# Performance work log

Measured on AMD Instinct MI355X. Metric: run time of the kernel, lower is better.

Reference implementation:

```python
import jax, jax.numpy as jnp
import numpy as np
import math

D_MODEL = 2048
N_HEADS = 16
HEAD_DIM = D_MODEL // N_HEADS
ROPE_THETA = 10000.0
EPS = 1e-5


def _rope_cos_sin(seq_len, dim, theta):
    inv_freq = 1.0 / theta ** (jnp.arange(0, dim, 2, dtype=jnp.float32) / dim)  # [dim/2]
    t = jnp.arange(seq_len, dtype=jnp.float32)
    freqs = jnp.outer(t, inv_freq)  # [S, dim/2]
    return jnp.cos(freqs), jnp.sin(freqs)


def _apply_rope(x, cos, sin):
    # x: [B, S, H, D]; pairs (even, odd) rotated by angle freqs[s, d/2]
    xs = x.reshape(x.shape[:-1] + (x.shape[-1] // 2, 2))
    x0, x1 = xs[..., 0], xs[..., 1]
    c = cos[None, :, None, :]
    s = sin[None, :, None, :]
    out = jnp.stack([x0 * c - x1 * s, x0 * s + x1 * c], axis=-1)
    return out.reshape(x.shape)


def _layernorm(x, w, eps):
    # LayerNorm over last dim, no bias
    mu = jnp.mean(x, axis=-1, keepdims=True)
    var = jnp.mean(jnp.square(x - mu), axis=-1, keepdims=True)
    return (x - mu) * jax.lax.rsqrt(var + eps) * w


def setup_inputs() -> dict:
    key = jax.random.key(0)
    ks = jax.random.split(key, 5)
    B, S = 2, 2048
    w_std = math.sqrt(1.0 / D_MODEL)  # ~xavier for square matrices
    return {
        "x": jax.random.normal(ks[0], (B, S, D_MODEL), dtype=jnp.float32),
        "wq": jax.random.normal(ks[1], (D_MODEL, D_MODEL), dtype=jnp.float32) * w_std,
        "wk": jax.random.normal(ks[2], (D_MODEL, D_MODEL), dtype=jnp.float32) * w_std,
        "wv": jax.random.normal(ks[3], (D_MODEL, D_MODEL), dtype=jnp.float32) * w_std,
        "wo": jax.random.normal(ks[4], (D_MODEL, D_MODEL), dtype=jnp.float32) * w_std,
        "q_norm_w": jnp.ones((HEAD_DIM,), dtype=jnp.float32),
        "k_norm_w": jnp.ones((HEAD_DIM,), dtype=jnp.float32),
        "window_size": 1024,
    }


def reference(x, wq, wk, wv, wo, q_norm_w, k_norm_w, window_size):
    B, S, _ = x.shape
    # bias-free projections (torch Linear: x @ W.T)
    q = (x @ wq.T).reshape(B, S, N_HEADS, HEAD_DIM)
    k = (x @ wk.T).reshape(B, S, N_HEADS, HEAD_DIM)
    v = (x @ wv.T).reshape(B, S, N_HEADS, HEAD_DIM)

    cos, sin = _rope_cos_sin(S, HEAD_DIM, ROPE_THETA)
    q = _apply_rope(q, cos, sin)
    k = _apply_rope(k, cos, sin)

    # per-head QK LayerNorm (no bias)
    q = _layernorm(q, q_norm_w, EPS)
    k = _layernorm(k, k_norm_w, EPS)

    scale = 1.0 / math.sqrt(HEAD_DIM)
    scores = jnp.einsum("bqhd,bkhd->bhqk", q, k) * scale  # [B,H,S,S]

    # sliding-window causal mask: attend to j in [i - window, i]
    i = jnp.arange(S)[:, None]
    j = jnp.arange(S)[None, :]
    allowed = (j <= i) & (j >= i - window_size)
    scores = jnp.where(allowed, scores, -jnp.inf)

    attn = jax.nn.softmax(scores, axis=-1)
    out = jnp.einsum("bhqk,bkhd->bqhd", attn, v).reshape(B, S, D_MODEL)
    return out @ wo.T
```

## Files before the change

### kernel.cpp

```cpp
#include <hip/hip_runtime.h>

typedef __bf16 bfv8 __attribute__((ext_vector_type(8)));
typedef float f32x4 __attribute__((ext_vector_type(4)));

#define DMODEL 2048
#define NHEADS 16
#define HEADD 128
#define SEQ 2048
#define BATCH 2
#define MROWS (BATCH * SEQ)

__device__ __forceinline__ unsigned short f2bf(float f) {
    unsigned int x = __float_as_uint(f);
    x += 0x7fffu + ((x >> 16) & 1u);
    return (unsigned short)(x >> 16);
}
__device__ __forceinline__ unsigned int pk2(float a, float b) {
    return (unsigned int)f2bf(a) | ((unsigned int)f2bf(b) << 16);
}

__global__ __launch_bounds__(256) void cvt_all(const float* __restrict__ x,
                                               const float* __restrict__ wq,
                                               const float* __restrict__ wk,
                                               const float* __restrict__ wv,
                                               const float* __restrict__ wo,
                                               unsigned short* __restrict__ dst) {
    int bid = blockIdx.x;
    const float* s;
    int off;
    if (bid < 8192)       { s = x;  off = bid; }
    else if (bid < 12288) { s = wq; off = bid - 8192; }
    else if (bid < 16384) { s = wk; off = bid - 12288; }
    else if (bid < 20480) { s = wv; off = bid - 16384; }
    else                  { s = wo; off = bid - 20480; }
    int i = off * 1024 + threadIdx.x * 4;
    float4 v = *(const float4*)(s + i);
    ushort4 o;
    o.x = f2bf(v.x); o.y = f2bf(v.y); o.z = f2bf(v.z); o.w = f2bf(v.w);
    *(ushort4*)(dst + (size_t)bid * 1024 + threadIdx.x * 4) = o;
}

template <int CPRL, int ITERS>
__device__ __forceinline__ void stage_n(const unsigned short* __restrict__ gbase,
                                        unsigned short* lds, size_t strideShorts,
                                        int wave, int lane) {
#pragma unroll
    for (int i = 0; i < ITERS; ++i) {
        int L = wave * (64 * ITERS) + i * 64 + lane;
        int m = L >> CPRL, c = L & ((1 << CPRL) - 1);
        int g = c ^ (m & 7);
        const unsigned short* gp = gbase + (size_t)m * strideShorts + g * 8;
        __builtin_amdgcn_global_load_lds(
            (const __attribute__((address_space(1))) unsigned int*)gp,
            (__attribute__((address_space(3))) unsigned int*)(lds + (size_t)(wave * (64 * ITERS) + i * 64) * 8),
            16, 0, 0);
    }
}

#define GBK 64

__global__ __launch_bounds__(256, 4) void gemm_qkv(const unsigned short* __restrict__ A,
                                                   const unsigned short* __restrict__ Bw,
                                                   unsigned short* __restrict__ Qb,
                                                   unsigned short* __restrict__ Kb,
                                                   unsigned short* __restrict__ VT,
                                                   const float* __restrict__ qnw,
                                                   const float* __restrict__ knw) {
    __shared__ __align__(16) unsigned short As[128 * 64];
    __shared__ __align__(16) unsigned short Bs[128 * 64];
    const int K = DMODEL;
    int tid  = threadIdx.x;
    int bm   = blockIdx.y * 128, bn = blockIdx.x * 128;
    int wave = tid >> 6, lane = tid & 63;
    int wm   = (wave >> 1) * 64, wn = (wave & 1) * 64;
    int lr   = lane & 15, lg = lane >> 4;

    f32x4 acc[4][4];
    f32x4 z = {0.f, 0.f, 0.f, 0.f};
#pragma unroll
    for (int i = 0; i < 4; ++i)
#pragma unroll
        for (int j = 0; j < 4; ++j) acc[i][j] = z;

    const unsigned short* Ab = A  + (size_t)bm * K;
    const unsigned short* Bb = Bw + (size_t)bn * K;

    for (int k0 = 0; k0 < K; k0 += GBK) {
        __syncthreads();
        stage_n<3, 4>(Ab + k0, As, K, wave, lane);
        stage_n<3, 4>(Bb + k0, Bs, K, wave, lane);
        __syncthreads();
#pragma unroll
        for (int kk = 0; kk < GBK; kk += 32) {
            int ck = (kk >> 3) + lg;
            bfv8 af[4], bf[4];
#pragma unroll
            for (int i = 0; i < 4; ++i)
                af[i] = *(const bfv8*)&As[(wm + i * 16 + lr) * 64 + (ck ^ (lr & 7)) * 8];
#pragma unroll
            for (int j = 0; j < 4; ++j)
                bf[j] = *(const bfv8*)&Bs[(wn + j * 16 + lr) * 64 + (ck ^ (lr & 7)) * 8];
#pragma unroll
            for (int i = 0; i < 4; ++i)
#pragma unroll
                for (int j = 0; j < 4; ++j)
                    acc[i][j] = __builtin_amdgcn_mfma_f32_16x16x32_bf16(af[i], bf[j], acc[i][j], 0, 0, 0);
        }
    }
    int lm = lr;
    int region = bn >> 11;
    int nloc   = bn & 2047;
    if (region < 2) {
        unsigned short* C = region ? Kb : Qb;
        const float* nw = region ? knw : qnw;
        float scale = region ? 1.0f : 0.08838834764831845f;
        float invf[4], wnw[4];
#pragma unroll
        for (int j = 0; j < 4; ++j) {
            int dd = wn + j * 16 + lm;
            invf[j] = exp2f(-(float)(dd >> 1) * 0.20762050593046f);
            wnw[j] = nw[dd];
        }
        int sbase = (bm & (SEQ - 1)) + wm + lg * 4;
#pragma unroll
        for (int i = 0; i < 4; ++i)
#pragma unroll
            for (int r = 0; r < 4; ++r) {
                float sv = (float)(sbase + i * 16 + r);
#pragma unroll
                for (int j = 0; j < 4; ++j) {
                    float sn, cs;
                    __sincosf(sv * invf[j], &sn, &cs);
                    float x0 = acc[i][j][r];
                    float x1 = __shfl_xor(x0, 1);
                    acc[i][j][r] = (lm & 1) ? fmaf(x1, sn, x0 * cs)
                                            : fmaf(x0, cs, -(x1 * sn));
                }
            }
        float* red = (float*)As;
        int half = wn >> 6;
        __syncthreads();
#pragma unroll
        for (int i = 0; i < 4; ++i)
#pragma unroll
            for (int r = 0; r < 4; ++r) {
                float a0 = acc[i][0][r], a1 = acc[i][1][r], a2 = acc[i][2][r], a3 = acc[i][3][r];
                float s1 = (a0 + a1) + (a2 + a3);
                float s2 = fmaf(a0, a0, fmaf(a1, a1, fmaf(a2, a2, a3 * a3)));
#pragma unroll
                for (int msk = 1; msk <= 8; msk <<= 1) {
                    s1 += __shfl_xor(s1, msk);
                    s2 += __shfl_xor(s2, msk);
                }
                if (lm == 0) {
                    int rloc = wm + lg * 4 + i * 16 + r;
                    red[(rloc * 2 + half) * 2 + 0] = s1;
                    red[(rloc * 2 + half) * 2 + 1] = s2;
                }
            }
        __syncthreads();
#pragma unroll
        for (int i = 0; i < 4; ++i)
#pragma unroll
            for (int r = 0; r < 4; ++r) {
                int rloc = wm + lg * 4 + i * 16 + r;
                float t1 = red[(rloc * 2 + 0) * 2 + 0] + red[(rloc * 2 + 1) * 2 + 0];
                float t2 = red[(rloc * 2 + 0) * 2 + 1] + red[(rloc * 2 + 1) * 2 + 1];
                float mu  = t1 * (1.0f / 128.0f);
                float var = t2 * (1.0f / 128.0f) - mu * mu;
                float rs  = rsqrtf(var + 1e-5f) * scale;
                size_t rowoff = (size_t)(bm + rloc) * DMODEL + nloc;
#pragma unroll
                for (int j = 0; j < 4; ++j)
                    C[rowoff + wn + j * 16 + lm] = f2bf((acc[i][j][r] - mu) * rs * wnw[j]);
            }
    } else {
        int orow0 = bm + wm + lg * 4;
#pragma unroll
        for (int i = 0; i < 4; ++i) {
            int row = orow0 + i * 16;
            int bb = row >> 11, ss = row & (SEQ - 1);
#pragma unroll
            for (int j = 0; j < 4; ++j) {
                int col = nloc + wn + j * 16 + lm;
                int hh = col >> 7, dd = col & (HEADD - 1);
                ushort4 o4;
                o4.x = f2bf(acc[i][j][0]);
                o4.y = f2bf(acc[i][j][1]);
                o4.z = f2bf(acc[i][j][2]);
                o4.w = f2bf(acc[i][j][3]);
                *(ushort4*)(VT + ((size_t)((bb * NHEADS + hh) * HEADD + dd)) * SEQ + ss) = o4;
            }
        }
    }
}

__global__ __launch_bounds__(256) void gemm_bt(const unsigned short* __restrict__ A,
                                               const unsigned short* __restrict__ Bw,
                                               float* __restrict__ C,
                                               int M, int N, int K) {
    __shared__ __align__(16) unsigned short As[128 * 64];
    __shared__ __align__(16) unsigned short Bs[128 * 64];
    int tid  = threadIdx.x;
    int bm   = blockIdx.y * 128, bn = blockIdx.x * 128;
    int wave = tid >> 6, lane = tid & 63;
    int wm   = (wave >> 1) * 64, wn = (wave & 1) * 64;
    int lr   = lane & 15, lg = lane >> 4;

    f32x4 acc[4][4];
    f32x4 z = {0.f, 0.f, 0.f, 0.f};
#pragma unroll
    for (int i = 0; i < 4; ++i)
#pragma unroll
        for (int j = 0; j < 4; ++j) acc[i][j] = z;

    const unsigned short* Ab = A  + (size_t)bm * K;
    const unsigned short* Bb = Bw + (size_t)bn * K;

    for (int k0 = 0; k0 < K; k0 += GBK) {
        __syncthreads();
        stage_n<3, 4>(Ab + k0, As, K, wave, lane);
        stage_n<3, 4>(Bb + k0, Bs, K, wave, lane);
        __syncthreads();
#pragma unroll
        for (int kk = 0; kk < GBK; kk += 32) {
            int ck = (kk >> 3) + lg;
            bfv8 af[4], bf[4];
#pragma unroll
            for (int i = 0; i < 4; ++i)
                af[i] = *(const bfv8*)&As[(wm + i * 16 + lr) * 64 + (ck ^ (lr & 7)) * 8];
#pragma unroll
            for (int j = 0; j < 4; ++j)
                bf[j] = *(const bfv8*)&Bs[(wn + j * 16 + lr) * 64 + (ck ^ (lr & 7)) * 8];
#pragma unroll
            for (int i = 0; i < 4; ++i)
#pragma unroll
                for (int j = 0; j < 4; ++j)
                    acc[i][j] = __builtin_amdgcn_mfma_f32_16x16x32_bf16(af[i], bf[j], acc[i][j], 0, 0, 0);
        }
    }
    int orow0 = bm + wm + lg * 4;
    int ocol0 = bn + wn + lr;
#pragma unroll
    for (int i = 0; i < 4; ++i)
#pragma unroll
        for (int j = 0; j < 4; ++j)
#pragma unroll
            for (int r = 0; r < 4; ++r)
                C[(size_t)(orow0 + i * 16 + r) * N + ocol0 + j * 16] = acc[i][j][r];
}

#define AQT 128
#define AKT 128

__global__ __launch_bounds__(256, 2) void attn_mfma(const unsigned short* __restrict__ qb,
                                                    const unsigned short* __restrict__ kb,
                                                    const unsigned short* __restrict__ vt,
                                                    unsigned short* __restrict__ ob,
                                                    const int* __restrict__ wptr) {
    __shared__ __align__(16) unsigned short Ks[128 * 128];
    __shared__ __align__(16) unsigned short Ps[4 * 32 * 128];
    int tid  = threadIdx.x;
    int wq   = tid >> 6, lane = tid & 63;
    int lm   = lane & 15, lg = lane >> 4;
    int lm7  = lm & 7;
    int gid  = blockIdx.x;
    int xcd  = gid & 7, slot = gid >> 3;
    int bh   = xcd * 4 + (slot >> 4);
    int b    = bh >> 4, h = bh & 15;
    int q0   = (15 - (slot & 15)) * AQT;
    int W    = *wptr;
    unsigned short* PsW = &Ps[wq * 32 * 128];

    bfv8 qa[2][4];
#pragma unroll
    for (int nq = 0; nq < 2; ++nq) {
        const unsigned short* qp = qb + (size_t)(b * SEQ + q0 + wq * 32 + nq * 16 + lm) * DMODEL + h * HEADD + lg * 8;
#pragma unroll
        for (int kk = 0; kk < 4; ++kk) qa[nq][kk] = *(const bfv8*)(qp + kk * 32);
    }

    f32x4 o[2][8];
    f32x4 z = {0.f, 0.f, 0.f, 0.f};
#pragma unroll
    for (int mq = 0; mq < 2; ++mq)
#pragma unroll
        for (int n = 0; n < 8; ++n) o[mq][n] = z;
    float mrow[2] = {-1e30f, -1e30f}, lrow[2] = {0.f, 0.f};

    const unsigned short* kbase = kb + (size_t)(b * SEQ) * DMODEL + h * HEADD;
    const unsigned short* vbase = vt + (size_t)((b * NHEADS + h) * HEADD) * SEQ;

    int kt_lo = max(0, q0 - W) & ~(AKT - 1);
    int qi0 = q0 + wq * 32 + lm;

    for (int kt = kt_lo; kt < q0 + AQT; kt += AKT) {
        __syncthreads();
        stage_n<4, 8>(kbase + (size_t)kt * DMODEL, Ks, DMODEL, wq, lane);
        __syncthreads();

        f32x4 s[8][2];
#pragma unroll
        for (int j = 0; j < 8; ++j) { s[j][0] = z; s[j][1] = z; }
#pragma unroll
        for (int kk = 0; kk < 4; ++kk)
#pragma unroll
            for (int j = 0; j < 8; ++j) {
                bfv8 af = *(const bfv8*)&Ks[(j * 16 + lm) * 128 + (((kk * 4 + lg)) ^ lm7) * 8];
                s[j][0] = __builtin_amdgcn_mfma_f32_16x16x32_bf16(af, qa[0][kk], s[j][0], 0, 0, 0);
                s[j][1] = __builtin_amdgcn_mfma_f32_16x16x32_bf16(af, qa[1][kk], s[j][1], 0, 0, 0);
            }
        if ((kt + AKT - 1 > q0) || (kt < q0 + AQT - 1 - W)) {
#pragma unroll
            for (int j = 0; j < 8; ++j) {
                int kj0 = kt + j * 16 + lg * 4;
#pragma unroll
                for (int nq = 0; nq < 2; ++nq) {
                    int qi = qi0 + nq * 16;
#pragma unroll
                    for (int r = 0; r < 4; ++r) {
                        bool ok = (kj0 + r <= qi) && (kj0 + r >= qi - W);
                        s[j][nq][r] = ok ? s[j][nq][r] : -1e30f;
                    }
                }
            }
        }
        float alpha[2];
#pragma unroll
        for (int nq = 0; nq < 2; ++nq) {
            float mx = -1e30f;
#pragma unroll
            for (int j = 0; j < 8; ++j)
#pragma unroll
                for (int r = 0; r < 4; ++r) mx = fmaxf(mx, s[j][nq][r]);
            mx = fmaxf(mx, __shfl_xor(mx, 16));
            mx = fmaxf(mx, __shfl_xor(mx, 32));
            float mnew = fmaxf(mrow[nq], mx);
            alpha[nq] = __expf(mrow[nq] - mnew);
            mrow[nq] = mnew;
            float ls = 0.f;
#pragma unroll
            for (int j = 0; j < 8; ++j) {
                float p0 = __expf(s[j][nq][0] - mnew);
                float p1 = __expf(s[j][nq][1] - mnew);
                float p2 = __expf(s[j][nq][2] - mnew);
                float p3 = __expf(s[j][nq][3] - mnew);
                ls += (p0 + p1) + (p2 + p3);
                int c0 = (j * 2 + (lg >> 1)) ^ lm7;
                uint2 wv;
                wv.x = pk2(p0, p1);
                wv.y = pk2(p2, p3);
                *(uint2*)&PsW[(nq * 16 + lm) * 128 + c0 * 8 + (lg & 1) * 4] = wv;
            }
            ls += __shfl_xor(ls, 16);
            ls += __shfl_xor(ls, 32);
            lrow[nq] = lrow[nq] * alpha[nq] + ls;
        }
#pragma unroll
        for (int mq = 0; mq < 2; ++mq)
#pragma unroll
            for (int r = 0; r < 4; ++r) {
                float al = __shfl(alpha[mq], lg * 4 + r);
#pragma unroll
                for (int n = 0; n < 8; ++n) o[mq][n][r] *= al;
            }
#pragma unroll
        for (int k2 = 0; k2 < 4; ++k2) {
            int cc = (k2 * 4 + lg) ^ lm7;
            bfv8 pa0 = *(const bfv8*)&PsW[lm * 128 + cc * 8];
            bfv8 pa1 = *(const bfv8*)&PsW[(16 + lm) * 128 + cc * 8];
            bfv8 vf[8];
#pragma unroll
            for (int n = 0; n < 8; ++n)
                vf[n] = *(const bfv8*)(vbase + (size_t)(n * 16 + lm) * SEQ + kt + (k2 * 4 + lg) * 8);
#pragma unroll
            for (int n = 0; n < 8; ++n) {
                o[0][n] = __builtin_amdgcn_mfma_f32_16x16x32_bf16(pa0, vf[n], o[0][n], 0, 0, 0);
                o[1][n] = __builtin_amdgcn_mfma_f32_16x16x32_bf16(pa1, vf[n], o[1][n], 0, 0, 0);
            }
        }
    }
#pragma unroll
    for (int mq = 0; mq < 2; ++mq) {
        float linv[4];
#pragma unroll
        for (int r = 0; r < 4; ++r) linv[r] = 1.0f / __shfl(lrow[mq], lg * 4 + r);
        int qrow = q0 + wq * 32 + mq * 16 + lg * 4;
        unsigned short* op = ob + (size_t)(b * SEQ + qrow) * DMODEL + h * HEADD + lm;
#pragma unroll
        for (int n = 0; n < 8; ++n)
#pragma unroll
            for (int r = 0; r < 4; ++r)
                op[(size_t)r * DMODEL + n * 16] = f2bf(o[mq][n][r] * linv[r]);
    }
}

extern "C" void kernel_launch(void* const* d_in, const int* in_sizes, int n_in,
                              void* d_out, int out_size, void* d_ws, size_t ws_size,
                              hipStream_t stream) {
    const float* x   = (const float*)d_in[0];
    const float* wq  = (const float*)d_in[1];
    const float* wk  = (const float*)d_in[2];
    const float* wv  = (const float*)d_in[3];
    const float* wo  = (const float*)d_in[4];
    const float* qnw = (const float*)d_in[5];
    const float* knw = (const float*)d_in[6];
    const int*   wsz = (const int*)d_in[7];
    float* out = (float*)d_out;

    char* ws = (char*)d_ws;
    unsigned short* xb  = (unsigned short*)(ws);
    unsigned short* w1  = (unsigned short*)(ws + 16777216);
    unsigned short* w4  = (unsigned short*)(ws + 41943040);
    unsigned short* qbf = (unsigned short*)(ws + 50331648);
    unsigned short* kbf = (unsigned short*)(ws + 67108864);
    unsigned short* vtb = (unsigned short*)(ws + 83886080);

    cvt_all<<<24576, 256, 0, stream>>>(x, wq, wk, wv, wo, xb);

    gemm_qkv<<<dim3(3 * DMODEL / 128, MROWS / 128), 256, 0, stream>>>(xb, w1, qbf, kbf, vtb, qnw, knw);

    attn_mfma<<<(SEQ / AQT) * NHEADS * BATCH, 256, 0, stream>>>(qbf, kbf, vtb, xb, wsz);

    gemm_bt<<<dim3(DMODEL / 128, MROWS / 128), 256, 0, stream>>>(xb, w4, out, MROWS, DMODEL, DMODEL);
}
```

Measured before the change: 444.8 us.

## Shrink attention tiles to 64 and stage V through LDS

The attention kernel moves from 128x128 query/key tiles with 32 query rows per wave to 64x64 tiles with 16 rows per wave. This doubles the grid and lowers per-thread register pressure. V tiles are now loaded into shared memory with async global-to-LDS copies instead of per-lane strided global reads, and the occupancy hints in launch_bounds are dropped for both the QKV GEMM and attention. The cost is more K/V reloads per query (half the reuse), more loop iterations and barriers, and possibly lower occupancy for the GEMM without the minimum-blocks hint.

```diff
diff --git a/kernel.cpp b/kernel.cpp
--- a/kernel.cpp
+++ b/kernel.cpp
@@ -59,13 +59,13 @@
 
 #define GBK 64
 
-__global__ __launch_bounds__(256, 4) void gemm_qkv(const unsigned short* __restrict__ A,
-                                                   const unsigned short* __restrict__ Bw,
-                                                   unsigned short* __restrict__ Qb,
-                                                   unsigned short* __restrict__ Kb,
-                                                   unsigned short* __restrict__ VT,
-                                                   const float* __restrict__ qnw,
-                                                   const float* __restrict__ knw) {
+__global__ __launch_bounds__(256) void gemm_qkv(const unsigned short* __restrict__ A,
+                                                const unsigned short* __restrict__ Bw,
+                                                unsigned short* __restrict__ Qb,
+                                                unsigned short* __restrict__ Kb,
+                                                unsigned short* __restrict__ VT,
+                                                const float* __restrict__ qnw,
+                                                const float* __restrict__ knw) {
     __shared__ __align__(16) unsigned short As[128 * 64];
     __shared__ __align__(16) unsigned short Bs[128 * 64];
     const int K = DMODEL;
@@ -250,149 +250,132 @@
                 C[(size_t)(orow0 + i * 16 + r) * N + ocol0 + j * 16] = acc[i][j][r];
 }
 
-#define AQT 128
-#define AKT 128
-
-__global__ __launch_bounds__(256, 2) void attn_mfma(const unsigned short* __restrict__ qb,
-                                                    const unsigned short* __restrict__ kb,
-                                                    const unsigned short* __restrict__ vt,
-                                                    unsigned short* __restrict__ ob,
-                                                    const int* __restrict__ wptr) {
-    __shared__ __align__(16) unsigned short Ks[128 * 128];
-    __shared__ __align__(16) unsigned short Ps[4 * 32 * 128];
+#define AQT 64
+#define AKT 64
+
+__global__ __launch_bounds__(256) void attn_mfma(const unsigned short* __restrict__ qb,
+                                                 const unsigned short* __restrict__ kb,
+                                                 const unsigned short* __restrict__ vt,
+                                                 unsigned short* __restrict__ ob,
+                                                 const int* __restrict__ wptr) {
+    __shared__ __align__(16) unsigned short Ks[64 * 128];
+    __shared__ __align__(16) unsigned short Vs[128 * 64];
+    __shared__ __align__(16) unsigned short Ps[4 * 16 * 64];
     int tid  = threadIdx.x;
     int wq   = tid >> 6, lane = tid & 63;
     int lm   = lane & 15, lg = lane >> 4;
     int lm7  = lm & 7;
     int gid  = blockIdx.x;
     int xcd  = gid & 7, slot = gid >> 3;
-    int bh   = xcd * 4 + (slot >> 4);
+    int bh   = xcd * 4 + (slot >> 5);
     int b    = bh >> 4, h = bh & 15;
-    int q0   = (15 - (slot & 15)) * AQT;
+    int q0   = (31 - (slot & 31)) * AQT;
     int W    = *wptr;
-    unsigned short* PsW = &Ps[wq * 32 * 128];
-
-    bfv8 qa[2][4];
-#pragma unroll
-    for (int nq = 0; nq < 2; ++nq) {
-        const unsigned short* qp = qb + (size_t)(b * SEQ + q0 + wq * 32 + nq * 16 + lm) * DMODEL + h * HEADD + lg * 8;
-#pragma unroll
-        for (int kk = 0; kk < 4; ++kk) qa[nq][kk] = *(const bfv8*)(qp + kk * 32);
-    }
-
-    f32x4 o[2][8];
+    unsigned short* PsW = &Ps[wq * 1024];
+
+    bfv8 qa[4];
+    {
+        const unsigned short* qp = qb + (size_t)(b * SEQ + q0 + wq * 16 + lm) * DMODEL + h * HEADD + lg * 8;
+#pragma unroll
+        for (int kk = 0; kk < 4; ++kk) qa[kk] = *(const bfv8*)(qp + kk * 32);
+    }
+
+    f32x4 o[8];
     f32x4 z = {0.f, 0.f, 0.f, 0.f};
 #pragma unroll
-    for (int mq = 0; mq < 2; ++mq)
-#pragma unroll
-        for (int n = 0; n < 8; ++n) o[mq][n] = z;
-    float mrow[2] = {-1e30f, -1e30f}, lrow[2] = {0.f, 0.f};
+    for (int n = 0; n < 8; ++n) o[n] = z;
+    float mrow = -1e30f, lrow = 0.f;
 
     const unsigned short* kbase = kb + (size_t)(b * SEQ) * DMODEL + h * HEADD;
     const unsigned short* vbase = vt + (size_t)((b * NHEADS + h) * HEADD) * SEQ;
 
     int kt_lo = max(0, q0 - W) & ~(AKT - 1);
-    int qi0 = q0 + wq * 32 + lm;
+    int qi = q0 + wq * 16 + lm;
 
     for (int kt = kt_lo; kt < q0 + AQT; kt += AKT) {
         __syncthreads();
-        stage_n<4, 8>(kbase + (size_t)kt * DMODEL, Ks, DMODEL, wq, lane);
-        __syncthreads();
-
-        f32x4 s[8][2];
-#pragma unroll
-        for (int j = 0; j < 8; ++j) { s[j][0] = z; s[j][1] = z; }
-#pragma unroll
-        for (int kk = 0; kk < 4; ++kk)
-#pragma unroll
-            for (int j = 0; j < 8; ++j) {
-                bfv8 af = *(const bfv8*)&Ks[(j * 16 + lm) * 128 + (((kk * 4 + lg)) ^ lm7) * 8];
-                s[j][0] = __builtin_amdgcn_mfma_f32_16x16x32_bf16(af, qa[0][kk], s[j][0], 0, 0, 0);
-                s[j][1] = __builtin_amdgcn_mfma_f32_16x16x32_bf16(af, qa[1][kk], s[j][1], 0, 0, 0);
-            }
-        if ((kt + AKT - 1 > q0) || (kt < q0 + AQT - 1 - W)) {
-#pragma unroll
-            for (int j = 0; j < 8; ++j) {
+        stage_n<4, 4>(kbase + (size_t)kt * DMODEL, Ks, DMODEL, wq, lane);
+        stage_n<3, 4>(vbase + kt, Vs, SEQ, wq, lane);
+        __syncthreads();
+
+        f32x4 s[4];
+#pragma unroll
+        for (int j = 0; j < 4; ++j) s[j] = z;
+#pragma unroll
+        for (int kk = 0; kk < 4; ++kk) {
+#pragma unroll
+            for (int j = 0; j < 4; ++j) {
+                int ck = (kk * 4 + lg) ^ lm7;
+                bfv8 af = *(const bfv8*)&Ks[(j * 16 + lm) * 128 + ck * 8];
+                s[j] = __builtin_amdgcn_mfma_f32_16x16x32_bf16(af, qa[kk], s[j], 0, 0, 0);
+            }
+        }
+        if ((kt + 63 >= q0) || (kt < q0 + 63 - W)) {
+#pragma unroll
+            for (int j = 0; j < 4; ++j) {
                 int kj0 = kt + j * 16 + lg * 4;
 #pragma unroll
-                for (int nq = 0; nq < 2; ++nq) {
-                    int qi = qi0 + nq * 16;
-#pragma unroll
-                    for (int r = 0; r < 4; ++r) {
-                        bool ok = (kj0 + r <= qi) && (kj0 + r >= qi - W);
-                        s[j][nq][r] = ok ? s[j][nq][r] : -1e30f;
-                    }
+                for (int r = 0; r < 4; ++r) {
+                    bool ok = (kj0 + r <= qi) && (kj0 + r >= qi - W);
+                    s[j][r] = ok ? s[j][r] : -1e30f;
                 }
             }
         }
-        float alpha[2];
-#pragma unroll
-        for (int nq = 0; nq < 2; ++nq) {
-            float mx = -1e30f;
-#pragma unroll
-            for (int j = 0; j < 8; ++j)
-#pragma unroll
-                for (int r = 0; r < 4; ++r) mx = fmaxf(mx, s[j][nq][r]);
-            mx = fmaxf(mx, __shfl_xor(mx, 16));
-            mx = fmaxf(mx, __shfl_xor(mx, 32));
-            float mnew = fmaxf(mrow[nq], mx);
-            alpha[nq] = __expf(mrow[nq] - mnew);
-            mrow[nq] = mnew;
-            float ls = 0.f;
-#pragma unroll
-            for (int j = 0; j < 8; ++j) {
-                float p0 = __expf(s[j][nq][0] - mnew);
-                float p1 = __expf(s[j][nq][1] - mnew);
-                float p2 = __expf(s[j][nq][2] - mnew);
-                float p3 = __expf(s[j][nq][3] - mnew);
-                ls += (p0 + p1) + (p2 + p3);
-                int c0 = (j * 2 + (lg >> 1)) ^ lm7;
-                uint2 wv;
-                wv.x = pk2(p0, p1);
-                wv.y = pk2(p2, p3);
-                *(uint2*)&PsW[(nq * 16 + lm) * 128 + c0 * 8 + (lg & 1) * 4] = wv;
-            }
-            ls += __shfl_xor(ls, 16);
-            ls += __shfl_xor(ls, 32);
-            lrow[nq] = lrow[nq] * alpha[nq] + ls;
-        }
-#pragma unroll
-        for (int mq = 0; mq < 2; ++mq)
-#pragma unroll
-            for (int r = 0; r < 4; ++r) {
-                float al = __shfl(alpha[mq], lg * 4 + r);
-#pragma unroll
-                for (int n = 0; n < 8; ++n) o[mq][n][r] *= al;
-            }
-#pragma unroll
-        for (int k2 = 0; k2 < 4; ++k2) {
+        float mx = -1e30f;
+#pragma unroll
+        for (int j = 0; j < 4; ++j)
+#pragma unroll
+            for (int r = 0; r < 4; ++r) mx = fmaxf(mx, s[j][r]);
+        mx = fmaxf(mx, __shfl_xor(mx, 16));
+        mx = fmaxf(mx, __shfl_xor(mx, 32));
+        float mnew  = fmaxf(mrow, mx);
+        float alpha = __expf(mrow - mnew);
+        mrow = mnew;
+        float ls = 0.f;
+#pragma unroll
+        for (int j = 0; j < 4; ++j) {
+            float p0 = __expf(s[j][0] - mnew);
+            float p1 = __expf(s[j][1] - mnew);
+            float p2 = __expf(s[j][2] - mnew);
+            float p3 = __expf(s[j][3] - mnew);
+            ls += (p0 + p1) + (p2 + p3);
+            int c0 = (j * 2 + (lg >> 1)) ^ lm7;
+            uint2 wv;
+            wv.x = pk2(p0, p1);
+            wv.y = pk2(p2, p3);
+            *(uint2*)&PsW[lm * 64 + c0 * 8 + (lg & 1) * 4] = wv;
+        }
+        ls += __shfl_xor(ls, 16);
+        ls += __shfl_xor(ls, 32);
+        lrow = lrow * alpha + ls;
+        float al[4];
+#pragma unroll
+        for (int r = 0; r < 4; ++r) al[r] = __shfl(alpha, lg * 4 + r);
+#pragma unroll
+        for (int n = 0; n < 8; ++n)
+#pragma unroll
+            for (int r = 0; r < 4; ++r) o[n][r] *= al[r];
+#pragma unroll
+        for (int k2 = 0; k2 < 2; ++k2) {
             int cc = (k2 * 4 + lg) ^ lm7;
-            bfv8 pa0 = *(const bfv8*)&PsW[lm * 128 + cc * 8];
-            bfv8 pa1 = *(const bfv8*)&PsW[(16 + lm) * 128 + cc * 8];
-            bfv8 vf[8];
-#pragma unroll
-            for (int n = 0; n < 8; ++n)
-                vf[n] = *(const bfv8*)(vbase + (size_t)(n * 16 + lm) * SEQ + kt + (k2 * 4 + lg) * 8);
+            bfv8 pa = *(const bfv8*)&PsW[lm * 64 + cc * 8];
 #pragma unroll
             for (int n = 0; n < 8; ++n) {
-                o[0][n] = __builtin_amdgcn_mfma_f32_16x16x32_bf16(pa0, vf[n], o[0][n], 0, 0, 0);
-                o[1][n] = __builtin_amdgcn_mfma_f32_16x16x32_bf16(pa1, vf[n], o[1][n], 0, 0, 0);
-            }
-        }
-    }
-#pragma unroll
-    for (int mq = 0; mq < 2; ++mq) {
-        float linv[4];
-#pragma unroll
-        for (int r = 0; r < 4; ++r) linv[r] = 1.0f / __shfl(lrow[mq], lg * 4 + r);
-        int qrow = q0 + wq * 32 + mq * 16 + lg * 4;
-        unsigned short* op = ob + (size_t)(b * SEQ + qrow) * DMODEL + h * HEADD + lm;
-#pragma unroll
-        for (int n = 0; n < 8; ++n)
-#pragma unroll
-            for (int r = 0; r < 4; ++r)
-                op[(size_t)r * DMODEL + n * 16] = f2bf(o[mq][n][r] * linv[r]);
-    }
+                bfv8 vf = *(const bfv8*)&Vs[(n * 16 + lm) * 64 + cc * 8];
+                o[n] = __builtin_amdgcn_mfma_f32_16x16x32_bf16(pa, vf, o[n], 0, 0, 0);
+            }
+        }
+    }
+    float linv[4];
+#pragma unroll
+    for (int r = 0; r < 4; ++r) linv[r] = 1.0f / __shfl(lrow, lg * 4 + r);
+    int qrow = q0 + wq * 16 + lg * 4;
+    unsigned short* op = ob + (size_t)(b * SEQ + qrow) * DMODEL + h * HEADD + lm;
+#pragma unroll
+    for (int n = 0; n < 8; ++n)
+#pragma unroll
+        for (int r = 0; r < 4; ++r)
+            op[(size_t)r * DMODEL + n * 16] = f2bf(o[n][r] * linv[r]);
 }
 
 extern "C" void kernel_launch(void* const* d_in, const int* in_sizes, int n_in,
```

Measured after the change: 485.7 us. 1.09x slower.
